# Performance work log

Hardware: AMD Instinct MI355X
Metric: run time of the kernel (lower is better)

## Reference

```python
import jax, jax.numpy as jnp
import numpy as np

N = 50000
E = 500000
HID = 128
H = 4
D = HID // H
NUM_EDGE_TYPES = 8
EPS_LN = 1e-5


def setup_inputs() -> dict:
    key = jax.random.key(0)
    ks = jax.random.split(key, 16)
    s = 1.0 / np.sqrt(HID)
    return {
        "node_embeddings": jax.random.normal(ks[0], (N, HID), jnp.float32),
        "edge_index": jax.random.randint(ks[1], (2, E), 0, N, jnp.int32),
        "edge_type": jax.random.randint(ks[2], (E,), 0, NUM_EDGE_TYPES, jnp.int32),
        "task_embedding": jax.random.normal(ks[3], (HID,), jnp.float32),
        "W_src": jax.random.normal(ks[4], (HID, HID), jnp.float32) * s,
        "b_src": jnp.zeros((HID,), jnp.float32),
        "W_dst": jax.random.normal(ks[5], (HID, HID), jnp.float32) * s,
        "b_dst": jnp.zeros((HID,), jnp.float32),
        "edge_emb": jax.random.normal(ks[6], (NUM_EDGE_TYPES, HID), jnp.float32),
        "att": jax.random.normal(ks[7], (H, D), jnp.float32) * s,
        "W_out": jax.random.normal(ks[8], (HID, HID), jnp.float32) * s,
        "b_out": jnp.zeros((HID,), jnp.float32),
        "norm_w": jnp.ones((HID,), jnp.float32),
        "norm_b": jnp.zeros((HID,), jnp.float32),
        "W_film": jax.random.normal(ks[9], (HID, 2 * HID), jnp.float32) * s,
        "b_film": jnp.zeros((2 * HID,), jnp.float32),
    }


def reference(node_embeddings, edge_index, edge_type, task_embedding,
              W_src, b_src, W_dst, b_dst, edge_emb, att,
              W_out, b_out, norm_w, norm_b, W_film, b_film):
    num_nodes = node_embeddings.shape[0]
    src, dst = edge_index[0], edge_index[1]

    # Node projections -> [N, H, D]
    x_src = (node_embeddings @ W_src + b_src).reshape(num_nodes, H, D)
    x_dst = (node_embeddings @ W_dst + b_dst).reshape(num_nodes, H, D)
    e = edge_emb[edge_type].reshape(-1, H, D)  # [E, H, D]

    # GATv2 attention logits per edge per head
    combined = jax.nn.leaky_relu(x_src[src] + x_dst[dst] + e, negative_slope=0.2)
    logits = jnp.einsum('ehd,hd->eh', combined, att)  # [E, H]

    # Scatter-softmax over destination nodes
    mx = jax.ops.segment_max(logits, dst, num_segments=num_nodes)  # [N, H]
    mx = jnp.where(jnp.isinf(mx), jnp.zeros_like(mx), mx)
    ex = jnp.exp(logits - mx[dst])
    sums = jax.ops.segment_sum(ex, dst, num_segments=num_nodes)  # [N, H]
    attn = ex / jnp.maximum(sums[dst], 1e-12)  # [E, H]

    # Weighted message aggregation
    msg = x_src[src] * attn[..., None]  # [E, H, D]
    agg = jax.ops.segment_sum(msg, dst, num_segments=num_nodes)  # [N, H, D]
    agg = agg.reshape(num_nodes, HID) @ W_out + b_out

    # Task FiLM modulation
    film = task_embedding @ W_film + b_film  # [2*HID]
    gamma, beta = film[:HID], film[HID:]
    agg = agg * (1.0 + 0.5 * jnp.tanh(gamma))[None, :] + beta[None, :]

    # Residual + LayerNorm
    y = node_embeddings + agg
    mu = jnp.mean(y, axis=-1, keepdims=True)
    var = jnp.mean((y - mu) ** 2, axis=-1, keepdims=True)
    return (y - mu) / jnp.sqrt(var + EPS_LN) * norm_w + norm_b
```

## Files before the change

### kernel.cpp

```cpp
#include <hip/hip_runtime.h>
#include <hip/hip_bf16.h>

#define N_NODES 50000
#define E_EDGES 500000
#define HID 128
#define NHEAD 4
#define HDIM 32
#define SCAN_BLOCKS ((N_NODES + 255) / 256)

typedef __attribute__((ext_vector_type(8))) short bf16x8;
typedef __attribute__((ext_vector_type(4))) float f32x4;

static __device__ __forceinline__ float b2f(unsigned short u) {
    return __uint_as_float((unsigned int)u << 16);
}
static __device__ __forceinline__ unsigned short f2b(float f) {
    unsigned int u = __float_as_uint(f);
    u += 0x7FFFu + ((u >> 16) & 1u);
    return (unsigned short)(u >> 16);
}

__global__ __launch_bounds__(256) void film_kernel(
    const float* __restrict__ task, const float* __restrict__ Wf,
    const float* __restrict__ bf, float* __restrict__ film)
{
    __shared__ float tsk[HID];
    const int t = threadIdx.x;
    if (t < HID) tsk[t] = task[t];
    __syncthreads();
    float acc = bf[t];
    #pragma unroll 8
    for (int k = 0; k < HID; ++k)
        acc = fmaf(tsk[k], Wf[k * 256 + t], acc);
    if (t < HID) film[t] = 1.f + 0.5f * tanhf(acc);
    else         film[t] = acc;
}

__global__ __launch_bounds__(256) void prep_weights(
    const float* __restrict__ Ws, const float* __restrict__ Wd,
    short* __restrict__ B1)
{
    const int id = blockIdx.x * 256 + threadIdx.x;
    const int n = id >> 7;
    const int k = id & 127;
    const float v = (n < HID) ? Ws[(size_t)k * HID + n]
                              : Wd[(size_t)k * HID + (n - HID)];
    B1[(size_t)n * HID + k] = (short)f2b(v);
}

__global__ __launch_bounds__(256) void gemm_mfma(
    const float* __restrict__ A, const short* __restrict__ B1,
    const float* __restrict__ bs, const float* __restrict__ bd,
    unsigned short* __restrict__ xs, unsigned short* __restrict__ xd)
{
    __shared__ unsigned short a_lds[64 * HID];
    const int t  = threadIdx.x;
    const int nb = blockIdx.x * 64;

    #pragma unroll
    for (int i = 0; i < 8; ++i) {
        const int f   = t + 256 * i;
        const int row = f >> 5;
        const int k4  = f & 31;
        const int node = nb + row;
        float4 v;
        if (node < N_NODES) v = *(const float4*)(A + (size_t)node * HID + k4 * 4);
        else { v.x = v.y = v.z = v.w = 0.f; }
        ushort4 h;
        h.x = f2b(v.x); h.y = f2b(v.y); h.z = f2b(v.z); h.w = f2b(v.w);
        int byte = row * 256 + k4 * 8;
        byte ^= (row & 7) << 4;
        *(ushort4*)((char*)a_lds + byte) = h;
    }
    __syncthreads();

    const int w   = t >> 6;
    const int l   = t & 63;
    const int l15 = l & 15;
    const int kg  = l >> 4;
    const int r   = w * 16 + l15;

    f32x4 acc[16];
    #pragma unroll
    for (int nf = 0; nf < 16; ++nf) acc[nf] = (f32x4){0.f, 0.f, 0.f, 0.f};

    #pragma unroll
    for (int ks = 0; ks < 4; ++ks) {
        int abyte = r * 256 + ks * 64 + kg * 16;
        abyte ^= (r & 7) << 4;
        const bf16x8 a = *(const bf16x8*)((char*)a_lds + abyte);
        #pragma unroll
        for (int nf = 0; nf < 16; ++nf) {
            const bf16x8 b = *(const bf16x8*)(
                B1 + (size_t)(nf * 16 + l15) * HID + ks * 32 + kg * 8);
            acc[nf] = __builtin_amdgcn_mfma_f32_16x16x32_bf16(a, b, acc[nf], 0, 0, 0);
        }
    }

    #pragma unroll
    for (int nf = 0; nf < 16; ++nf) {
        const int col = nf * 16 + l15;
        const bool is_src = (col < HID);
        const float bias = is_src ? bs[col] : bd[col - HID];
        #pragma unroll
        for (int j = 0; j < 4; ++j) {
            const int node = nb + w * 16 + kg * 4 + j;
            if (node < N_NODES) {
                const unsigned short us = f2b(acc[nf][j] + bias);
                if (is_src) xs[(size_t)node * HID + col] = us;
                else        xd[(size_t)node * HID + (col - HID)] = us;
            }
        }
    }
}

__global__ __launch_bounds__(256) void hist_kernel(
    const int* __restrict__ ei, int* __restrict__ deg)
{
    const int e = blockIdx.x * 256 + threadIdx.x;
    if (e < E_EDGES) atomicAdd(&deg[ei[E_EDGES + e]], 1);
}

__global__ __launch_bounds__(256) void reduce_blocks(
    const int* __restrict__ deg, int* __restrict__ blocksum)
{
    __shared__ int ws_[4];
    const int t = threadIdx.x;
    const int i = blockIdx.x * 256 + t;
    int v = (i < N_NODES) ? deg[i] : 0;
    #pragma unroll
    for (int off = 32; off; off >>= 1) v += __shfl_down(v, off);
    if ((t & 63) == 0) ws_[t >> 6] = v;
    __syncthreads();
    if (t == 0) blocksum[blockIdx.x] = ws_[0] + ws_[1] + ws_[2] + ws_[3];
}

__global__ __launch_bounds__(256) void scan_blocksums(
    const int* __restrict__ blocksum, int* __restrict__ blockoff,
    int* __restrict__ rowptr)
{
    __shared__ int wtot[4];
    const int t    = threadIdx.x;
    const int lane = t & 63;
    const int w    = t >> 6;
    int v = (t < SCAN_BLOCKS) ? blocksum[t] : 0;
    const int own = v;
    #pragma unroll
    for (int off = 1; off < 64; off <<= 1) {
        const int u = __shfl_up(v, off);
        if (lane >= off) v += u;
    }
    if (lane == 63) wtot[w] = v;
    __syncthreads();
    int woff = 0;
    #pragma unroll
    for (int k = 0; k < 4; ++k) if (k < w) woff += wtot[k];
    if (t < SCAN_BLOCKS) blockoff[t] = woff + v - own;
    if (t == 0) rowptr[N_NODES] = E_EDGES;
}

__global__ __launch_bounds__(256) void scan_within(
    const int* __restrict__ deg, const int* __restrict__ blockoff,
    int* __restrict__ rowptr, int* __restrict__ cursor)
{
    __shared__ int wtot[4];
    const int t    = threadIdx.x;
    const int lane = t & 63;
    const int w    = t >> 6;
    const int i    = blockIdx.x * 256 + t;
    int v = (i < N_NODES) ? deg[i] : 0;
    const int own = v;
    #pragma unroll
    for (int off = 1; off < 64; off <<= 1) {
        const int u = __shfl_up(v, off);
        if (lane >= off) v += u;
    }
    if (lane == 63) wtot[w] = v;
    __syncthreads();
    int woff = blockoff[blockIdx.x];
    #pragma unroll
    for (int k = 0; k < 4; ++k) if (k < w) woff += wtot[k];
    if (i < N_NODES) {
        const int ex = woff + v - own;
        rowptr[i] = ex;
        cursor[i] = ex;
    }
}

__global__ __launch_bounds__(256) void scatter_kernel(
    const int* __restrict__ ei, const int* __restrict__ et,
    int* __restrict__ cursor, int* __restrict__ pack)
{
    const int e = blockIdx.x * 256 + threadIdx.x;
    if (e < E_EDGES) {
        const int d = ei[E_EDGES + e];
        const int pos = atomicAdd(&cursor[d], 1);
        pack[pos] = ei[e] | (et[e] << 16);
    }
}

__global__ __launch_bounds__(256) void gather_agg(
    const int* __restrict__ rowptr, const int* __restrict__ pack,
    const unsigned short* __restrict__ xsrc,
    const unsigned short* __restrict__ xdst,
    const float* __restrict__ eemb, const float* __restrict__ att,
    float* __restrict__ agg)
{
    const int lane = threadIdx.x & 31;
    const int grp  = threadIdx.x >> 5;
    const int node = blockIdx.x * 8 + grp;
    if (node >= N_NODES) return;

    const float4 av = *(const float4*)(att + lane * 4);
    const ushort4 xdu = *(const ushort4*)(xdst + (size_t)node * HID + lane * 4);
    const float xdx = b2f(xdu.x), xdy = b2f(xdu.y),
                xdz = b2f(xdu.z), xdw = b2f(xdu.w);

    float a0 = 0.f, a1 = 0.f, a2 = 0.f, a3 = 0.f, sum = 0.f;
    const int b = rowptr[node];
    const int e = rowptr[node + 1];

    int i = b;
    for (; i + 1 < e; i += 2) {
        const int pk0 = pack[i];
        const int pk1 = pack[i + 1];
        const int s0 = pk0 & 0xFFFF, ty0 = pk0 >> 16;
        const int s1 = pk1 & 0xFFFF, ty1 = pk1 >> 16;
        const ushort4 u0 = *(const ushort4*)(xsrc + (size_t)s0 * HID + lane * 4);
        const float4  ev0 = *(const float4*)(eemb + (size_t)ty0 * HID + lane * 4);
        const ushort4 u1 = *(const ushort4*)(xsrc + (size_t)s1 * HID + lane * 4);
        const float4  ev1 = *(const float4*)(eemb + (size_t)ty1 * HID + lane * 4);
        const float x0x = b2f(u0.x), x0y = b2f(u0.y), x0z = b2f(u0.z), x0w = b2f(u0.w);
        const float x1x = b2f(u1.x), x1y = b2f(u1.y), x1z = b2f(u1.z), x1w = b2f(u1.w);
        float c, p0 = 0.f, p1 = 0.f;
        c = x0x + xdx + ev0.x; c = (c > 0.f) ? c : 0.2f * c; p0 = fmaf(c, av.x, p0);
        c = x0y + xdy + ev0.y; c = (c > 0.f) ? c : 0.2f * c; p0 = fmaf(c, av.y, p0);
        c = x0z + xdz + ev0.z; c = (c > 0.f) ? c : 0.2f * c; p0 = fmaf(c, av.z, p0);
        c = x0w + xdw + ev0.w; c = (c > 0.f) ? c : 0.2f * c; p0 = fmaf(c, av.w, p0);
        c = x1x + xdx + ev1.x; c = (c > 0.f) ? c : 0.2f * c; p1 = fmaf(c, av.x, p1);
        c = x1y + xdy + ev1.y; c = (c > 0.f) ? c : 0.2f * c; p1 = fmaf(c, av.y, p1);
        c = x1z + xdz + ev1.z; c = (c > 0.f) ? c : 0.2f * c; p1 = fmaf(c, av.z, p1);
        c = x1w + xdw + ev1.w; c = (c > 0.f) ? c : 0.2f * c; p1 = fmaf(c, av.w, p1);
        p0 += __shfl_xor(p0, 1); p1 += __shfl_xor(p1, 1);
        p0 += __shfl_xor(p0, 2); p1 += __shfl_xor(p1, 2);
        p0 += __shfl_xor(p0, 4); p1 += __shfl_xor(p1, 4);
        const float ex0 = expf(p0);
        const float ex1 = expf(p1);
        a0 = fmaf(ex0, x0x, a0); a1 = fmaf(ex0, x0y, a1);
        a2 = fmaf(ex0, x0z, a2); a3 = fmaf(ex0, x0w, a3);
        a0 = fmaf(ex1, x1x, a0); a1 = fmaf(ex1, x1y, a1);
        a2 = fmaf(ex1, x1z, a2); a3 = fmaf(ex1, x1w, a3);
        sum += ex0 + ex1;
    }
    if (i < e) {
        const int pk0 = pack[i];
        const int s0 = pk0 & 0xFFFF, ty0 = pk0 >> 16;
        const ushort4 u0 = *(const ushort4*)(xsrc + (size_t)s0 * HID + lane * 4);
        const float4  ev0 = *(const float4*)(eemb + (size_t)ty0 * HID + lane * 4);
        const float x0x = b2f(u0.x), x0y = b2f(u0.y), x0z = b2f(u0.z), x0w = b2f(u0.w);
        float c, p0 = 0.f;
        c = x0x + xdx + ev0.x; c = (c > 0.f) ? c : 0.2f * c; p0 = fmaf(c, av.x, p0);
        c = x0y + xdy + ev0.y; c = (c > 0.f) ? c : 0.2f * c; p0 = fmaf(c, av.y, p0);
        c = x0z + xdz + ev0.z; c = (c > 0.f) ? c : 0.2f * c; p0 = fmaf(c, av.z, p0);
        c = x0w + xdw + ev0.w; c = (c > 0.f) ? c : 0.2f * c; p0 = fmaf(c, av.w, p0);
        p0 += __shfl_xor(p0, 1);
        p0 += __shfl_xor(p0, 2);
        p0 += __shfl_xor(p0, 4);
        const float ex0 = expf(p0);
        a0 = fmaf(ex0, x0x, a0); a1 = fmaf(ex0, x0y, a1);
        a2 = fmaf(ex0, x0z, a2); a3 = fmaf(ex0, x0w, a3);
        sum += ex0;
    }

    const float inv = 1.f / fmaxf(sum, 1e-12f);
    float4 o;
    o.x = a0 * inv; o.y = a1 * inv; o.z = a2 * inv; o.w = a3 * inv;
    *(float4*)(agg + (size_t)node * HID + lane * 4) = o;
}

__global__ __launch_bounds__(256) void finalize(
    const float* __restrict__ agg,
    const float* __restrict__ A,   const float* __restrict__ Wo,
    const float* __restrict__ bo,  const float* __restrict__ film,
    const float* __restrict__ nw_, const float* __restrict__ nb_,
    float* __restrict__ out)
{
    __shared__ float a_tile[64][HID];
    const int t  = threadIdx.x;
    const int nb = blockIdx.x * 64;

    #pragma unroll
    for (int i = 0; i < 8; ++i) {
        int f  = t + 256 * i;
        int m  = f >> 5;
        int k4 = f & 31;
        int node = nb + m;
        float4 v;
        if (node < N_NODES) v = *(const float4*)(agg + (size_t)node * HID + k4 * 4);
        else { v.x = v.y = v.z = v.w = 0.f; }
        *(float4*)&a_tile[m][k4 * 4] = v;
    }
    __syncthreads();

    const int cg = t & 31;
    const int rg = t >> 5;
    const int cc = cg * 4;
    const int m0 = rg * 8;

    float acc[8][4];
    #pragma unroll
    for (int m = 0; m < 8; ++m)
        #pragma unroll
        for (int j = 0; j < 4; ++j) acc[m][j] = 0.f;

    for (int kc = 0; kc < 32; ++kc) {
        const int k0 = kc * 4;
        const float4 w0 = *(const float4*)(Wo + (size_t)(k0 + 0) * HID + cc);
        const float4 w1 = *(const float4*)(Wo + (size_t)(k0 + 1) * HID + cc);
        const float4 w2 = *(const float4*)(Wo + (size_t)(k0 + 2) * HID + cc);
        const float4 w3 = *(const float4*)(Wo + (size_t)(k0 + 3) * HID + cc);
        #pragma unroll
        for (int m = 0; m < 8; ++m) {
            const float4 av = *(const float4*)&a_tile[m0 + m][k0];
            acc[m][0] = fmaf(av.x, w0.x, acc[m][0]);
            acc[m][1] = fmaf(av.x, w0.y, acc[m][1]);
            acc[m][2] = fmaf(av.x, w0.z, acc[m][2]);
            acc[m][3] = fmaf(av.x, w0.w, acc[m][3]);
            acc[m][0] = fmaf(av.y, w1.x, acc[m][0]);
            acc[m][1] = fmaf(av.y, w1.y, acc[m][1]);
            acc[m][2] = fmaf(av.y, w1.z, acc[m][2]);
            acc[m][3] = fmaf(av.y, w1.w, acc[m][3]);
            acc[m][0] = fmaf(av.z, w2.x, acc[m][0]);
            acc[m][1] = fmaf(av.z, w2.y, acc[m][1]);
            acc[m][2] = fmaf(av.z, w2.z, acc[m][2]);
            acc[m][3] = fmaf(av.z, w2.w, acc[m][3]);
            acc[m][0] = fmaf(av.w, w3.x, acc[m][0]);
            acc[m][1] = fmaf(av.w, w3.y, acc[m][1]);
            acc[m][2] = fmaf(av.w, w3.z, acc[m][2]);
            acc[m][3] = fmaf(av.w, w3.w, acc[m][3]);
        }
    }

    const float4 bv  = *(const float4*)(bo   + cc);
    const float4 gfv = *(const float4*)(film + cc);
    const float4 btv = *(const float4*)(film + HID + cc);
    const float4 nwv = *(const float4*)(nw_  + cc);
    const float4 nbv = *(const float4*)(nb_  + cc);

    #pragma unroll
    for (int m = 0; m < 8; ++m) {
        const int node = nb + m0 + m;
        float4 y;
        float4 r;
        if (node < N_NODES) r = *(const float4*)(A + (size_t)node * HID + cc);
        else { r.x = r.y = r.z = r.w = 0.f; }
        y.x = fmaf(acc[m][0] + bv.x, gfv.x, btv.x) + r.x;
        y.y = fmaf(acc[m][1] + bv.y, gfv.y, btv.y) + r.y;
        y.z = fmaf(acc[m][2] + bv.z, gfv.z, btv.z) + r.z;
        y.w = fmaf(acc[m][3] + bv.w, gfv.w, btv.w) + r.w;

        float s1 = y.x + y.y + y.z + y.w;
        float s2 = y.x * y.x + y.y * y.y + y.z * y.z + y.w * y.w;
        #pragma unroll
        for (int off = 1; off < 32; off <<= 1) {
            s1 += __shfl_xor(s1, off);
            s2 += __shfl_xor(s2, off);
        }
        const float mu   = s1 * (1.f / 128.f);
        const float var  = s2 * (1.f / 128.f) - mu * mu;
        const float rsig = rsqrtf(var + 1e-5f);
        if (node < N_NODES) {
            float4 o;
            o.x = (y.x - mu) * rsig * nwv.x + nbv.x;
            o.y = (y.y - mu) * rsig * nwv.y + nbv.y;
            o.z = (y.z - mu) * rsig * nwv.z + nbv.z;
            o.w = (y.w - mu) * rsig * nwv.w + nbv.w;
            *(float4*)(out + (size_t)node * HID + cc) = o;
        }
    }
}

extern "C" void kernel_launch(void* const* d_in, const int* in_sizes, int n_in,
                              void* d_out, int out_size, void* d_ws, size_t ws_size,
                              hipStream_t stream)
{
    const float* node_emb = (const float*)d_in[0];
    const int*   edge_idx = (const int*)  d_in[1];
    const int*   edge_ty  = (const int*)  d_in[2];
    const float* task     = (const float*)d_in[3];
    const float* W_src    = (const float*)d_in[4];
    const float* b_src    = (const float*)d_in[5];
    const float* W_dst    = (const float*)d_in[6];
    const float* b_dst    = (const float*)d_in[7];
    const float* edge_emb = (const float*)d_in[8];
    const float* att      = (const float*)d_in[9];
    const float* W_out    = (const float*)d_in[10];
    const float* b_out    = (const float*)d_in[11];
    const float* norm_w   = (const float*)d_in[12];
    const float* norm_b   = (const float*)d_in[13];
    const float* W_film   = (const float*)d_in[14];
    const float* b_film   = (const float*)d_in[15];
    float* out = (float*)d_out;

    char* ws = (char*)d_ws;
    float* agg      = (float*)ws;                            ws += (size_t)N_NODES * HID * 4;
    float* film     = (float*)ws;                            ws += 256 * 4;
    int*   deg      = (int*)ws;                              ws += (size_t)N_NODES * 4;
    int*   rowptr   = (int*)ws;                              ws += (size_t)(N_NODES + 1) * 4;
    int*   cursor   = (int*)ws;                              ws += (size_t)N_NODES * 4;
    int*   blocksum = (int*)ws;                              ws += 256 * 4;
    int*   blockoff = (int*)ws;                              ws += 256 * 4;
    int*   pack     = (int*)ws;                              ws += (size_t)E_EDGES * 4;
    unsigned short* x_src = (unsigned short*)ws;             ws += (size_t)N_NODES * HID * 2;
    unsigned short* x_dst = (unsigned short*)ws;             ws += (size_t)N_NODES * HID * 2;
    short* wb1      = (short*)ws;                            ws += (size_t)256 * HID * 2;

    hipMemsetAsync(deg, 0, (size_t)N_NODES * sizeof(int), stream);

    film_kernel<<<1, 256, 0, stream>>>(task, W_film, b_film, film);
    hist_kernel<<<(E_EDGES + 255) / 256, 256, 0, stream>>>(edge_idx, deg);
    prep_weights<<<(256 * HID) / 256, 256, 0, stream>>>(W_src, W_dst, wb1);
    gemm_mfma<<<(N_NODES + 63) / 64, 256, 0, stream>>>(
        node_emb, wb1, b_src, b_dst, x_src, x_dst);
    reduce_blocks<<<SCAN_BLOCKS, 256, 0, stream>>>(deg, blocksum);
    scan_blocksums<<<1, 256, 0, stream>>>(blocksum, blockoff, rowptr);
    scan_within<<<SCAN_BLOCKS, 256, 0, stream>>>(deg, blockoff, rowptr, cursor);
    scatter_kernel<<<(E_EDGES + 255) / 256, 256, 0, stream>>>(
        edge_idx, edge_ty, cursor, pack);
    gather_agg<<<(N_NODES + 7) / 8, 256, 0, stream>>>(
        rowptr, pack, x_src, x_dst, edge_emb, att, agg);
    finalize<<<(N_NODES + 63) / 64, 256, 0, stream>>>(
        agg, node_emb, W_out, b_out, film, norm_w, norm_b, out);
}
```

Baseline: 290.0 us.

## Stage swizzled B in LDS, use 4x4 MFMA tiles, coalesce GEMM output stores

The projection GEMM now copies the whole pre-swizzled bf16 weight matrix into LDS (64 KB) instead of reading B fragments from global memory for every MFMA. Each wave now computes a 64x64 output tile with 4x4 fragments, which lets it reuse A and B fragments from registers. The epilogue goes through padded LDS so each store to x_src/x_dst is a 16-byte coalesced write rather than a scattered 2-byte write. The larger LDS footprint may reduce how many blocks fit on a CU, and every block reloads the full weight matrix.

```diff
diff --git a/kernel.cpp b/kernel.cpp
--- a/kernel.cpp
+++ b/kernel.cpp
@@ -9,6 +9,7 @@
 #define SCAN_BLOCKS ((N_NODES + 255) / 256)
 
 typedef __attribute__((ext_vector_type(8))) short bf16x8;
+typedef __attribute__((ext_vector_type(8))) unsigned short u16x8;
 typedef __attribute__((ext_vector_type(4))) float f32x4;
 
 static __device__ __forceinline__ float b2f(unsigned short u) {
@@ -38,22 +39,25 @@
 
 __global__ __launch_bounds__(256) void prep_weights(
     const float* __restrict__ Ws, const float* __restrict__ Wd,
-    short* __restrict__ B1)
+    unsigned short* __restrict__ B1)
 {
     const int id = blockIdx.x * 256 + threadIdx.x;
     const int n = id >> 7;
     const int k = id & 127;
     const float v = (n < HID) ? Ws[(size_t)k * HID + n]
                               : Wd[(size_t)k * HID + (n - HID)];
-    B1[(size_t)n * HID + k] = (short)f2b(v);
+    size_t byte = ((size_t)n * HID + k) * 2;
+    byte ^= (size_t)((n & 7) << 4);
+    *(unsigned short*)((char*)B1 + byte) = f2b(v);
 }
 
 __global__ __launch_bounds__(256) void gemm_mfma(
-    const float* __restrict__ A, const short* __restrict__ B1,
+    const float* __restrict__ A, const unsigned short* __restrict__ B1,
     const float* __restrict__ bs, const float* __restrict__ bd,
     unsigned short* __restrict__ xs, unsigned short* __restrict__ xd)
 {
     __shared__ unsigned short a_lds[64 * HID];
+    __shared__ unsigned short b_lds[256 * HID];
     const int t  = threadIdx.x;
     const int nb = blockIdx.x * 64;
 
@@ -72,44 +76,84 @@
         byte ^= (row & 7) << 4;
         *(ushort4*)((char*)a_lds + byte) = h;
     }
+    #pragma unroll
+    for (int i = 0; i < 16; ++i) {
+        const int off = (t + 256 * i) * 8;
+        const u16x8 v = *(const u16x8*)(B1 + off);
+        *(u16x8*)(b_lds + off) = v;
+    }
     __syncthreads();
 
     const int w   = t >> 6;
     const int l   = t & 63;
     const int l15 = l & 15;
     const int kg  = l >> 4;
-    const int r   = w * 16 + l15;
-
-    f32x4 acc[16];
-    #pragma unroll
-    for (int nf = 0; nf < 16; ++nf) acc[nf] = (f32x4){0.f, 0.f, 0.f, 0.f};
+
+    f32x4 acc[4][4];
+    #pragma unroll
+    for (int mf = 0; mf < 4; ++mf)
+        #pragma unroll
+        for (int nf = 0; nf < 4; ++nf) acc[mf][nf] = (f32x4){0.f, 0.f, 0.f, 0.f};
 
     #pragma unroll
     for (int ks = 0; ks < 4; ++ks) {
-        int abyte = r * 256 + ks * 64 + kg * 16;
-        abyte ^= (r & 7) << 4;
-        const bf16x8 a = *(const bf16x8*)((char*)a_lds + abyte);
-        #pragma unroll
-        for (int nf = 0; nf < 16; ++nf) {
-            const bf16x8 b = *(const bf16x8*)(
-                B1 + (size_t)(nf * 16 + l15) * HID + ks * 32 + kg * 8);
-            acc[nf] = __builtin_amdgcn_mfma_f32_16x16x32_bf16(a, b, acc[nf], 0, 0, 0);
-        }
-    }
-
-    #pragma unroll
-    for (int nf = 0; nf < 16; ++nf) {
-        const int col = nf * 16 + l15;
-        const bool is_src = (col < HID);
-        const float bias = is_src ? bs[col] : bd[col - HID];
-        #pragma unroll
-        for (int j = 0; j < 4; ++j) {
-            const int node = nb + w * 16 + kg * 4 + j;
-            if (node < N_NODES) {
-                const unsigned short us = f2b(acc[nf][j] + bias);
-                if (is_src) xs[(size_t)node * HID + col] = us;
-                else        xd[(size_t)node * HID + (col - HID)] = us;
+        bf16x8 af[4], bfg[4];
+        #pragma unroll
+        for (int mf = 0; mf < 4; ++mf) {
+            const int r = mf * 16 + l15;
+            int byte = r * 256 + ks * 64 + kg * 16;
+            byte ^= (r & 7) << 4;
+            af[mf] = *(const bf16x8*)((const char*)a_lds + byte);
+        }
+        #pragma unroll
+        for (int nf = 0; nf < 4; ++nf) {
+            const int rb = w * 64 + nf * 16 + l15;
+            int byte = rb * 256 + ks * 64 + kg * 16;
+            byte ^= (rb & 7) << 4;
+            bfg[nf] = *(const bf16x8*)((const char*)b_lds + byte);
+        }
+        #pragma unroll
+        for (int mf = 0; mf < 4; ++mf)
+            #pragma unroll
+            for (int nf = 0; nf < 4; ++nf)
+                acc[mf][nf] = __builtin_amdgcn_mfma_f32_16x16x32_bf16(
+                    af[mf], bfg[nf], acc[mf][nf], 0, 0, 0);
+    }
+
+    float bias[4];
+    #pragma unroll
+    for (int nf = 0; nf < 4; ++nf) {
+        const int col = w * 64 + nf * 16 + l15;
+        bias[nf] = (col < HID) ? bs[col] : bd[col - HID];
+    }
+
+    __syncthreads();
+    unsigned short* c_lds = b_lds;
+
+    #pragma unroll
+    for (int mf = 0; mf < 4; ++mf)
+        #pragma unroll
+        for (int nf = 0; nf < 4; ++nf) {
+            const int col = w * 64 + nf * 16 + l15;
+            #pragma unroll
+            for (int j = 0; j < 4; ++j) {
+                const int row = mf * 16 + kg * 4 + j;
+                c_lds[row * 264 + col] = f2b(acc[mf][nf][j] + bias[nf]);
             }
+        }
+    __syncthreads();
+
+    #pragma unroll
+    for (int p = 0; p < 8; ++p) {
+        const int row   = p * 8 + (t >> 5);
+        const int chunk = t & 31;
+        const int node  = nb + row;
+        if (node < N_NODES) {
+            const u16x8 v = *(const u16x8*)(c_lds + row * 264 + chunk * 8);
+            if (chunk < 16)
+                *(u16x8*)(xs + (size_t)node * HID + chunk * 8) = v;
+            else
+                *(u16x8*)(xd + (size_t)node * HID + (chunk - 16) * 8) = v;
         }
     }
 }
@@ -406,14 +450,14 @@
     float* agg      = (float*)ws;                            ws += (size_t)N_NODES * HID * 4;
     float* film     = (float*)ws;                            ws += 256 * 4;
     int*   deg      = (int*)ws;                              ws += (size_t)N_NODES * 4;
-    int*   rowptr   = (int*)ws;                              ws += (size_t)(N_NODES + 1) * 4;
+    int*   rowptr   = (int*)ws;                              ws += (size_t)(N_NODES + 4) * 4;
     int*   cursor   = (int*)ws;                              ws += (size_t)N_NODES * 4;
     int*   blocksum = (int*)ws;                              ws += 256 * 4;
     int*   blockoff = (int*)ws;                              ws += 256 * 4;
     int*   pack     = (int*)ws;                              ws += (size_t)E_EDGES * 4;
     unsigned short* x_src = (unsigned short*)ws;             ws += (size_t)N_NODES * HID * 2;
     unsigned short* x_dst = (unsigned short*)ws;             ws += (size_t)N_NODES * HID * 2;
-    short* wb1      = (short*)ws;                            ws += (size_t)256 * HID * 2;
+    unsigned short* wb1   = (unsigned short*)ws;             ws += (size_t)256 * HID * 2;
 
     hipMemsetAsync(deg, 0, (size_t)N_NODES * sizeof(int), stream);
 
```

Measured after the change: 255.8 us. -11.8%, faster.
